# Optimization experiments

Hardware: AMD Instinct MI355X
Metric: run time of the kernel (lower is better)

The kernel has to match this reference:

```python
import jax, jax.numpy as jnp
import numpy as np

BS, NQ, NC, NT = 64, 300, 10, 30
W_CLASS, W_BBOX, W_GIOU = 2.0, 5.0, 2.0


def cxcywh_to_xyxy(b):
    c, s = b[..., :2], b[..., 2:]
    return jnp.concatenate([c - 0.5 * s, c + 0.5 * s], axis=-1)


def _area(b):
    return (b[..., 2] - b[..., 0]) * (b[..., 3] - b[..., 1])


def giou_pairwise(a, b):
    # a: [N,4] xyxy, b: [M,4] xyxy -> [N,M]
    sum_area = _area(a)[:, None] + _area(b)[None, :]
    lt = jnp.maximum(a[:, None, :2], b[None, :, :2])
    rb = jnp.minimum(a[:, None, 2:], b[None, :, 2:])
    wh = jnp.clip(rb - lt, 0.0)
    inter = wh[..., 0] * wh[..., 1]
    union = sum_area - inter
    iou = inter / union
    ltc = jnp.minimum(a[:, None, :2], b[None, :, :2])
    rbc = jnp.maximum(a[:, None, 2:], b[None, :, 2:])
    whc = jnp.clip(rbc - ltc, 0.0)
    areac = whc[..., 0] * whc[..., 1]
    return iou - (areac - union) / areac


def giou_elementwise(a, b):
    # a, b: [N,4] xyxy -> [N]
    sum_area = _area(a) + _area(b)
    lt = jnp.maximum(a[..., :2], b[..., :2])
    rb = jnp.minimum(a[..., 2:], b[..., 2:])
    wh = jnp.clip(rb - lt, 0.0)
    inter = wh[..., 0] * wh[..., 1]
    union = sum_area - inter
    iou = inter / union
    ltc = jnp.minimum(a[..., :2], b[..., :2])
    rbc = jnp.maximum(a[..., 2:], b[..., 2:])
    whc = jnp.clip(rbc - ltc, 0.0)
    areac = whc[..., 0] * whc[..., 1]
    return iou - (areac - union) / areac


def hungarian(cost):
    # Exact rectangular assignment (Kuhn-Munkres with potentials), rows n <= cols m.
    # Returns (row_ind, col_ind) of the n matched pairs, equivalent to
    # scipy.optimize.linear_sum_assignment.
    n, m = cost.shape
    u = np.zeros(n + 1)
    v = np.zeros(m + 1)
    p = np.zeros(m + 1, dtype=np.int64)    # p[j] = row matched to col j (1-based)
    way = np.zeros(m + 1, dtype=np.int64)
    for i in range(1, n + 1):
        p[0] = i
        j0 = 0
        minv = np.full(m + 1, np.inf)
        used = np.zeros(m + 1, dtype=bool)
        while True:
            used[j0] = True
            i0 = p[j0]
            cur = cost[i0 - 1] - u[i0] - v[1:]
            mask = ~used[1:]
            better = mask & (cur < minv[1:])
            minv[1:] = np.where(better, cur, minv[1:])
            way[1:] = np.where(better, j0, way[1:])
            free = np.nonzero(mask)[0]
            j1 = free[np.argmin(minv[1:][free])] + 1
            delta = minv[j1]
            u[p[used]] += delta
            v[used] -= delta
            minv[~used] -= delta
            j0 = j1
            if p[j0] == 0:
                break
        while j0 != 0:
            j1 = way[j0]
            p[j0] = p[j1]
            j0 = j1
    rows = p[1:] - 1
    cols = np.arange(m)
    sel = rows >= 0
    return rows[sel], cols[sel]


def compute_match(pred_logits, pred_boxes, labels, boxes):
    # Mirrors @torch.no_grad() match(): build cost matrix on device, assign on host.
    bs, nq, _ = pred_logits.shape
    t = boxes.shape[1]
    out_prob = jax.nn.sigmoid(pred_logits).reshape(bs * nq, -1)
    out_bbox = pred_boxes.reshape(bs * nq, 4)
    tgt_ids = labels.reshape(-1)
    tgt_bbox = boxes.reshape(-1, 4)
    cost_class = -out_prob[:, tgt_ids]                                   # [bs*nq, bs*t]
    cost_bbox = jnp.sum(jnp.abs(out_bbox[:, None, :] - tgt_bbox[None, :, :]), -1)
    cost_giou = -giou_pairwise(cxcywh_to_xyxy(out_bbox), cxcywh_to_xyxy(tgt_bbox))
    C = W_BBOX * cost_bbox + W_CLASS * cost_class + W_GIOU * cost_giou
    C = np.asarray(jax.device_get(C), dtype=np.float64).reshape(bs, nq, bs * t)
    bidx, sidx, tidx = [], [], []
    for b in range(bs):
        block = C[b, :, b * t:(b + 1) * t]          # [nq, t]
        r, c = hungarian(block.T)                   # rows = targets, cols = queries
        bidx.extend([b] * len(c))
        sidx.extend(c.tolist())
        tidx.extend(r.tolist())
    return (np.asarray(bidx, np.int64), np.asarray(sidx, np.int64),
            np.asarray(tidx, np.int64))


def compute_loss(pred_logits, pred_boxes, labels, boxes, bidx, sidx, tidx):
    bs, nq, _ = pred_logits.shape
    num = max(1, len(bidx))
    target_classes = jnp.full((bs, nq), 10, dtype=jnp.int32)
    target_classes = target_classes.at[bidx, sidx].set(
        labels[bidx, tidx].astype(jnp.int32))
    onehot = jax.nn.one_hot(target_classes, 11, dtype=pred_logits.dtype)[..., :10]
    # sigmoid focal loss, alpha=0.25, gamma=2, reduction='sum'
    x, t = pred_logits, onehot
    p = jax.nn.sigmoid(x)
    ce = jnp.maximum(x, 0.0) - x * t + jnp.log1p(jnp.exp(-jnp.abs(x)))
    p_t = p * t + (1.0 - p) * (1.0 - t)
    alpha_t = 0.25 * t + 0.75 * (1.0 - t)
    loss_ce = jnp.sum(alpha_t * ce * (1.0 - p_t) ** 2) / num
    src_boxes = pred_boxes[bidx, sidx]
    tgt_boxes = boxes[bidx, tidx]
    loss_bbox = jnp.sum(jnp.abs(src_boxes - tgt_boxes)) / num
    g = giou_elementwise(cxcywh_to_xyxy(src_boxes), cxcywh_to_xyxy(tgt_boxes))
    loss_giou = jnp.sum(1.0 - g) / num
    return loss_ce + 5.0 * loss_bbox + 2.0 * loss_giou


def setup_inputs() -> dict:
    key = jax.random.key(0)
    k0, k1, k2, k3 = jax.random.split(key, 4)
    pred_logits = jax.random.normal(k0, (BS, NQ, NC), dtype=jnp.float32)
    pred_boxes = jax.random.uniform(k1, (BS, NQ, 4), dtype=jnp.float32)
    labels = jax.random.randint(k2, (BS, NT), 0, 10, dtype=jnp.int64)
    boxes = jax.random.uniform(k3, (BS, NT, 4), dtype=jnp.float32)
    return {"pred_logits": pred_logits, "pred_boxes": pred_boxes,
            "labels": labels, "boxes": boxes}


def reference(pred_logits, pred_boxes, labels, boxes):
    bidx, sidx, tidx = compute_match(pred_logits, pred_boxes, labels, boxes)
    return compute_loss(pred_logits, pred_boxes, labels, boxes, bidx, sidx, tidx)
```

## Files before the change

kernel.cpp:

```cpp
#include <hip/hip_runtime.h>
#include <math.h>

#define NQ 300
#define NQP 301
#define NT 30
#define NC 10
#define NTH 512
#define NWAVE 8
#define INFF 3.0e38f

__device__ __forceinline__ float sigf(float x){ return 1.0f/(1.0f + expf(-x)); }
__device__ __forceinline__ float softplusf(float x){ return fmaxf(x,0.0f) + log1pf(expf(-fabsf(x))); }

template<int CTRL,int RMASK>
__device__ __forceinline__ float dppmin_f(float x){
  int t = __builtin_amdgcn_update_dpp(0x7f800000, __float_as_int(x), CTRL, RMASK, 0xf, false);
  return fminf(x, __int_as_float(t));
}
template<int CTRL,int RMASK>
__device__ __forceinline__ unsigned dppmin_u(unsigned x){
  unsigned t = (unsigned)__builtin_amdgcn_update_dpp((int)0xFFFFFFFFu, (int)x, CTRL, RMASK, 0xf, false);
  return x < t ? x : t;
}
template<int CTRL,int RMASK>
__device__ __forceinline__ float dppadd_f(float x){
  int t = __builtin_amdgcn_update_dpp(0, __float_as_int(x), CTRL, RMASK, 0xf, false);
  return x + __int_as_float(t);
}
__device__ __forceinline__ void wave_argmin64(float v, unsigned idx, float &ov, int &oj){
  float x = v;
  x = dppmin_f<0x111,0xf>(x); x = dppmin_f<0x112,0xf>(x);
  x = dppmin_f<0x114,0xf>(x); x = dppmin_f<0x118,0xf>(x);
  x = dppmin_f<0x142,0xa>(x); x = dppmin_f<0x143,0xc>(x);
  float vmin = __int_as_float(__builtin_amdgcn_readlane(__float_as_int(x), 63));
  unsigned c = (v == vmin) ? idx : 0xFFFFFFFFu;
  c = dppmin_u<0x111,0xf>(c); c = dppmin_u<0x112,0xf>(c);
  c = dppmin_u<0x114,0xf>(c); c = dppmin_u<0x118,0xf>(c);
  c = dppmin_u<0x142,0xa>(c); c = dppmin_u<0x143,0xc>(c);
  oj = __builtin_amdgcn_readlane((int)c, 63);
  ov = vmin;
}
__device__ __forceinline__ float wave_sum64(float v){
  float x = v;
  x = dppadd_f<0x111,0xf>(x); x = dppadd_f<0x112,0xf>(x);
  x = dppadd_f<0x114,0xf>(x); x = dppadd_f<0x118,0xf>(x);
  x = dppadd_f<0x142,0xa>(x); x = dppadd_f<0x143,0xc>(x);
  return __int_as_float(__builtin_amdgcn_readlane(__float_as_int(x), 63));
}

__global__ __launch_bounds__(NTH) void hm_main(
    const float* __restrict__ logits,
    const float* __restrict__ pbox,
    const int*   __restrict__ labels,
    const float* __restrict__ tbox,
    float* __restrict__ out)
{
  const int b = blockIdx.x;
  const int tid = threadIdx.x;
  const int wv = tid >> 6, ln = tid & 63;

  __shared__ float D[NT*NQ];
  __shared__ float psmT[NC*NQP];
  __shared__ float qraw[NQ][4], qxy[NQ][4], qarea[NQ];
  __shared__ float traw[NT][4], txy[NT][4], tarea[NT];
  __shared__ int   tlab[NT];
  __shared__ float uu[NT+1];
  __shared__ int   pcol[NQ];
  __shared__ int   wayl[NQ];
  __shared__ int   rargm[NT];
  __shared__ float redw[NWAVE];

  const float4* pb4 = (const float4*)pbox;
  for (int q = tid; q < NQ; q += NTH) {
    float4 s = pb4[(size_t)b*NQ + q];
    qraw[q][0]=s.x; qraw[q][1]=s.y; qraw[q][2]=s.z; qraw[q][3]=s.w;
    float x0=s.x-0.5f*s.z, y0=s.y-0.5f*s.w, x1=s.x+0.5f*s.z, y1=s.y+0.5f*s.w;
    qxy[q][0]=x0; qxy[q][1]=y0; qxy[q][2]=x1; qxy[q][3]=y1;
    qarea[q]=(x1-x0)*(y1-y0);
  }
  if (tid < NT) {
    float4 s = ((const float4*)tbox)[(size_t)b*NT + tid];
    traw[tid][0]=s.x; traw[tid][1]=s.y; traw[tid][2]=s.z; traw[tid][3]=s.w;
    float x0=s.x-0.5f*s.z, y0=s.y-0.5f*s.w, x1=s.x+0.5f*s.z, y1=s.y+0.5f*s.w;
    txy[tid][0]=x0; txy[tid][1]=y0; txy[tid][2]=x1; txy[tid][3]=y1;
    tarea[tid]=(x1-x0)*(y1-y0);
    tlab[tid]=labels[b*NT + tid];
  }
  for (int j = tid; j < NQ; j += NTH) { pcol[j]=0; wayl[j]=0x7fffffff; }

  float tot = 0.f;
  for (int e = tid; e < NQ*NC; e += NTH) {
    float x = logits[(size_t)b*NQ*NC + e];
    float pr = sigf(x);
    int q = e / NC, c = e - q*NC;
    psmT[c*NQP + q] = pr;
    tot += 0.75f * softplusf(x) * pr * pr;
  }
  __syncthreads();

  for (int i = wv; i < NT; i += NWAVE) {
    const float t0=traw[i][0], t1=traw[i][1], t2=traw[i][2], t3=traw[i][3];
    const float x0=txy[i][0], y0=txy[i][1], x1=txy[i][2], y1=txy[i][3];
    const float ta=tarea[i]; const int lab=tlab[i];
    const float* prow = &psmT[lab*NQP];
    float bv=INFF; unsigned bj=0xFFFFFFFFu;
    #pragma unroll
    for (int k = 0; k < 5; ++k) {
      int q = ln + (k<<6);
      if (k < 4 || ln < (NQ-256)) {
        float cb = fabsf(qraw[q][0]-t0)+fabsf(qraw[q][1]-t1)
                 + fabsf(qraw[q][2]-t2)+fabsf(qraw[q][3]-t3);
        float lt0=fmaxf(qxy[q][0],x0), lt1=fmaxf(qxy[q][1],y0);
        float rb0=fminf(qxy[q][2],x1), rb1=fminf(qxy[q][3],y1);
        float iw=fmaxf(rb0-lt0,0.f), ih=fmaxf(rb1-lt1,0.f);
        float inter=iw*ih;
        float uni=qarea[q]+ta-inter;
        float iou=inter/uni;
        float c0=fminf(qxy[q][0],x0), c1=fminf(qxy[q][1],y0);
        float c2=fmaxf(qxy[q][2],x1), c3=fmaxf(qxy[q][3],y1);
        float cw=fmaxf(c2-c0,0.f), ch=fmaxf(c3-c1,0.f);
        float areac=cw*ch;
        float g=iou-(areac-uni)/areac;
        float dval = 5.f*cb - 2.f*prow[q] - 2.f*g;
        D[i*NQ+q] = dval;
        if (dval < bv) { bv=dval; bj=(unsigned)q; }
      }
    }
    float vmin; int jmin;
    wave_argmin64(bv, bj, vmin, jmin);
    if (ln == 0) { uu[i+1]=vmin; rargm[i]=jmin; }
  }
  __syncthreads();

  if (tid < 64) {
    const int lane = tid;
    float u_reg = (lane < NT) ? uu[lane+1] : 0.f;
    float vvr[5] = {0.f,0.f,0.f,0.f,0.f};
    const bool v4 = lane < (NQ - 256);
    int jm = (lane < NT) ? rargm[lane] : 0;
    bool winner = false;
    if (lane < NT) {
      atomicMin(&wayl[jm], lane);
      winner = (wayl[jm] == lane);
      if (winner) pcol[jm] = lane + 1;
    }
    unsigned freerows = (unsigned)__ballot(lane < NT && !winner);
    while (freerows) {
      int fr = __builtin_ctz(freerows); freerows &= (freerows - 1);
      const int it = fr + 1;
      float minvr[5] = {INFF,INFF,INFF,INFF,INFF};
      int   usedm = 0;
      bool  onpath = (lane == fr);
      int   j0 = -1, i0 = it, j1 = 0;
      for (;;) {
        float ui0 = __int_as_float(__builtin_amdgcn_readlane(__float_as_int(u_reg), i0-1));
        const float* Drow = &D[(i0-1)*NQ];
        float lval = INFF; unsigned lidx = 0xFFFFFFFFu;
        #pragma unroll
        for (int k = 0; k < 5; ++k) {
          int c = lane + (k<<6);
          if ((k < 4 || v4) && !((usedm>>k)&1)) {
            float cur = Drow[c] - ui0 - vvr[k];
            if (cur < minvr[k]) { minvr[k] = cur; wayl[c] = j0; }
            if (minvr[k] < lval) { lval = minvr[k]; lidx = (unsigned)c; }
          }
        }
        float delta; int j1i;
        wave_argmin64(lval, lidx, delta, j1i);
        j1 = j1i;
        if (onpath) u_reg += delta;
        #pragma unroll
        for (int k = 0; k < 5; ++k) {
          if ((usedm>>k)&1) vvr[k]  -= delta;
          else              minvr[k] -= delta;
        }
        int pj1 = pcol[j1];
        if (pj1 == 0) break;
        onpath = onpath || (lane == (pj1-1));
        if (lane == (j1 & 63)) usedm |= (1 << (j1 >> 6));
        j0 = j1; i0 = pj1;
      }
      int j = j1;
      for (;;) {
        int jp = wayl[j];
        int rr = (jp < 0) ? it : pcol[jp];
        pcol[j] = rr;
        if (jp < 0) break;
        j = jp;
      }
    }
  }
  __syncthreads();

  if (tid < NQ) {
    int row = pcol[tid];
    if (row > 0) {
      int ti = row-1, q = tid;
      float l1 = fabsf(qraw[q][0]-traw[ti][0]) + fabsf(qraw[q][1]-traw[ti][1])
               + fabsf(qraw[q][2]-traw[ti][2]) + fabsf(qraw[q][3]-traw[ti][3]);
      float lt0=fmaxf(qxy[q][0],txy[ti][0]), lt1=fmaxf(qxy[q][1],txy[ti][1]);
      float rb0=fminf(qxy[q][2],txy[ti][2]), rb1=fminf(qxy[q][3],txy[ti][3]);
      float iw=fmaxf(rb0-lt0,0.f), ih=fmaxf(rb1-lt1,0.f);
      float inter=iw*ih;
      float uni=qarea[q]+tarea[ti]-inter;
      float iou=inter/uni;
      float c0=fminf(qxy[q][0],txy[ti][0]), c1=fminf(qxy[q][1],txy[ti][1]);
      float c2=fmaxf(qxy[q][2],txy[ti][2]), c3=fmaxf(qxy[q][3],txy[ti][3]);
      float cw=fmaxf(c2-c0,0.f), ch=fmaxf(c3-c1,0.f);
      float areac=cw*ch;
      float g=iou-(areac-uni)/areac;
      float x  = logits[((size_t)b*NQ+q)*NC + tlab[ti]];
      float pr = psmT[tlab[ti]*NQP + q];
      float sp = softplusf(x);
      float term0 = 0.75f*sp*pr*pr;
      float term1 = 0.25f*(sp - x)*(1.f-pr)*(1.f-pr);
      tot += (term1 - term0) + 5.f*l1 + 2.f*(1.f-g);
    }
  }
  float wsum = wave_sum64(tot);
  if (ln == 0) redw[wv] = wsum;
  __syncthreads();
  if (tid == 0) {
    float s = 0.f;
    #pragma unroll
    for (int w = 0; w < NWAVE; ++w) s += redw[w];
    atomicAdd(out, s * (1.0f/1920.0f));
  }
}

extern "C" void kernel_launch(void* const* d_in, const int* in_sizes, int n_in,
                              void* d_out, int out_size, void* d_ws, size_t ws_size,
                              hipStream_t stream) {
  const float* logits = (const float*)d_in[0];
  const float* pbox   = (const float*)d_in[1];
  const int*   labels = (const int*)d_in[2];
  const float* tbox   = (const float*)d_in[3];
  hipMemsetAsync(d_out, 0, sizeof(float), stream);
  hm_main<<<dim3(64), dim3(NTH), 0, stream>>>(logits, pbox, labels, tbox, (float*)d_out);
}
```

Measured before the change: 27.10 us.

## Keep Hungarian column state and query boxes in registers instead of LDS

Query boxes are now loaded straight into per-lane registers (five slots per lane) rather than staged in shared memory. The single-wave Hungarian solver keeps the column-to-row assignment and back-pointer arrays in registers, reading them across lanes with readlane. This is meant to remove LDS round-trips from the serial augmenting-path loop, which dominates latency. The costs are higher register pressure and switch-based slot selection, and the final loss pass is remapped so each wave handles one query slot.

```diff
diff --git a/kernel.cpp b/kernel.cpp
--- a/kernel.cpp
+++ b/kernel.cpp
@@ -11,6 +11,12 @@
 
 __device__ __forceinline__ float sigf(float x){ return 1.0f/(1.0f + expf(-x)); }
 __device__ __forceinline__ float softplusf(float x){ return fmaxf(x,0.0f) + log1pf(expf(-fabsf(x))); }
+__device__ __forceinline__ float readlane_f(float v, int l){
+  return __int_as_float(__builtin_amdgcn_readlane(__float_as_int(v), l));
+}
+__device__ __forceinline__ int readlane_i(int v, int l){
+  return __builtin_amdgcn_readlane(v, l);
+}
 
 template<int CTRL,int RMASK>
 __device__ __forceinline__ float dppmin_f(float x){
@@ -61,22 +67,27 @@
 
   __shared__ float D[NT*NQ];
   __shared__ float psmT[NC*NQP];
-  __shared__ float qraw[NQ][4], qxy[NQ][4], qarea[NQ];
   __shared__ float traw[NT][4], txy[NT][4], tarea[NT];
   __shared__ int   tlab[NT];
   __shared__ float uu[NT+1];
   __shared__ int   pcol[NQ];
-  __shared__ int   wayl[NQ];
+  __shared__ int   claimA[NQ];
   __shared__ int   rargm[NT];
   __shared__ float redw[NWAVE];
 
-  const float4* pb4 = (const float4*)pbox;
-  for (int q = tid; q < NQ; q += NTH) {
-    float4 s = pb4[(size_t)b*NQ + q];
-    qraw[q][0]=s.x; qraw[q][1]=s.y; qraw[q][2]=s.z; qraw[q][3]=s.w;
-    float x0=s.x-0.5f*s.z, y0=s.y-0.5f*s.w, x1=s.x+0.5f*s.z, y1=s.y+0.5f*s.w;
-    qxy[q][0]=x0; qxy[q][1]=y0; qxy[q][2]=x1; qxy[q][3]=y1;
-    qarea[q]=(x1-x0)*(y1-y0);
+  const bool v4 = ln < (NQ - 256);
+
+  float qcx[5],qcy[5],qw[5],qh[5],qx0[5],qy0[5],qx1[5],qy1[5],qar[5];
+  {
+    const float4* pb4 = (const float4*)pbox + (size_t)b*NQ;
+    #pragma unroll
+    for (int k = 0; k < 5; ++k) {
+      float4 s = (k < 4 || v4) ? pb4[ln + (k<<6)] : make_float4(0.f,0.f,0.f,0.f);
+      qcx[k]=s.x; qcy[k]=s.y; qw[k]=s.z; qh[k]=s.w;
+      qx0[k]=s.x-0.5f*s.z; qy0[k]=s.y-0.5f*s.w;
+      qx1[k]=s.x+0.5f*s.z; qy1[k]=s.y+0.5f*s.w;
+      qar[k]=(qx1[k]-qx0[k])*(qy1[k]-qy0[k]);
+    }
   }
   if (tid < NT) {
     float4 s = ((const float4*)tbox)[(size_t)b*NT + tid];
@@ -86,7 +97,7 @@
     tarea[tid]=(x1-x0)*(y1-y0);
     tlab[tid]=labels[b*NT + tid];
   }
-  for (int j = tid; j < NQ; j += NTH) { pcol[j]=0; wayl[j]=0x7fffffff; }
+  for (int j = tid; j < NQ; j += NTH) { pcol[j]=0; claimA[j]=0x7fffffff; }
 
   float tot = 0.f;
   for (int e = tid; e < NQ*NC; e += NTH) {
@@ -101,23 +112,22 @@
   for (int i = wv; i < NT; i += NWAVE) {
     const float t0=traw[i][0], t1=traw[i][1], t2=traw[i][2], t3=traw[i][3];
     const float x0=txy[i][0], y0=txy[i][1], x1=txy[i][2], y1=txy[i][3];
-    const float ta=tarea[i]; const int lab=tlab[i];
-    const float* prow = &psmT[lab*NQP];
+    const float ta=tarea[i];
+    const float* prow = &psmT[tlab[i]*NQP];
     float bv=INFF; unsigned bj=0xFFFFFFFFu;
     #pragma unroll
     for (int k = 0; k < 5; ++k) {
-      int q = ln + (k<<6);
-      if (k < 4 || ln < (NQ-256)) {
-        float cb = fabsf(qraw[q][0]-t0)+fabsf(qraw[q][1]-t1)
-                 + fabsf(qraw[q][2]-t2)+fabsf(qraw[q][3]-t3);
-        float lt0=fmaxf(qxy[q][0],x0), lt1=fmaxf(qxy[q][1],y0);
-        float rb0=fminf(qxy[q][2],x1), rb1=fminf(qxy[q][3],y1);
+      if (k < 4 || v4) {
+        int q = ln + (k<<6);
+        float cb = fabsf(qcx[k]-t0)+fabsf(qcy[k]-t1)+fabsf(qw[k]-t2)+fabsf(qh[k]-t3);
+        float lt0=fmaxf(qx0[k],x0), lt1=fmaxf(qy0[k],y0);
+        float rb0=fminf(qx1[k],x1), rb1=fminf(qy1[k],y1);
         float iw=fmaxf(rb0-lt0,0.f), ih=fmaxf(rb1-lt1,0.f);
         float inter=iw*ih;
-        float uni=qarea[q]+ta-inter;
+        float uni=qar[k]+ta-inter;
         float iou=inter/uni;
-        float c0=fminf(qxy[q][0],x0), c1=fminf(qxy[q][1],y0);
-        float c2=fmaxf(qxy[q][2],x1), c3=fmaxf(qxy[q][3],y1);
+        float c0=fminf(qx0[k],x0), c1=fminf(qy0[k],y0);
+        float c2=fmaxf(qx1[k],x1), c3=fmaxf(qy1[k],y1);
         float cw=fmaxf(c2-c0,0.f), ch=fmaxf(c3-c1,0.f);
         float areac=cw*ch;
         float g=iou-(areac-uni)/areac;
@@ -132,89 +142,125 @@
   }
   __syncthreads();
 
-  if (tid < 64) {
-    const int lane = tid;
+  if (wv == 0) {
+    const int lane = ln;
     float u_reg = (lane < NT) ? uu[lane+1] : 0.f;
-    float vvr[5] = {0.f,0.f,0.f,0.f,0.f};
-    const bool v4 = lane < (NQ - 256);
+    float vv0=0.f,vv1=0.f,vv2=0.f,vv3=0.f,vv4=0.f;
     int jm = (lane < NT) ? rargm[lane] : 0;
     bool winner = false;
     if (lane < NT) {
-      atomicMin(&wayl[jm], lane);
-      winner = (wayl[jm] == lane);
+      atomicMin(&claimA[jm], lane);
+      winner = (claimA[jm] == lane);
       if (winner) pcol[jm] = lane + 1;
     }
     unsigned freerows = (unsigned)__ballot(lane < NT && !winner);
+    int pc0=pcol[lane], pc1=pcol[lane+64], pc2=pcol[lane+128], pc3=pcol[lane+192];
+    int pc4 = v4 ? pcol[lane+256] : 0;
+    int wy0=0, wy1=0, wy2=0, wy3=0, wy4=0;
+
     while (freerows) {
       int fr = __builtin_ctz(freerows); freerows &= (freerows - 1);
       const int it = fr + 1;
-      float minvr[5] = {INFF,INFF,INFF,INFF,INFF};
-      int   usedm = 0;
-      bool  onpath = (lane == fr);
-      int   j0 = -1, i0 = it, j1 = 0;
+      float mn0=INFF,mn1=INFF,mn2=INFF,mn3=INFF,mn4=INFF;
+      int usedm = 0;
+      bool onpath = (lane == fr);
+      int j0 = -1, i0 = it, j1 = 0;
       for (;;) {
-        float ui0 = __int_as_float(__builtin_amdgcn_readlane(__float_as_int(u_reg), i0-1));
+        float ui0 = readlane_f(u_reg, i0-1);
         const float* Drow = &D[(i0-1)*NQ];
         float lval = INFF; unsigned lidx = 0xFFFFFFFFu;
-        #pragma unroll
-        for (int k = 0; k < 5; ++k) {
-          int c = lane + (k<<6);
-          if ((k < 4 || v4) && !((usedm>>k)&1)) {
-            float cur = Drow[c] - ui0 - vvr[k];
-            if (cur < minvr[k]) { minvr[k] = cur; wayl[c] = j0; }
-            if (minvr[k] < lval) { lval = minvr[k]; lidx = (unsigned)c; }
+        #define SCAN_K(K, MN, VV, WY) \
+          if ((K < 4 || v4) && !((usedm>>K)&1)) { \
+            float cur = Drow[lane + (K<<6)] - ui0 - VV; \
+            if (cur < MN) { MN = cur; WY = j0; } \
+            if (MN < lval) { lval = MN; lidx = (unsigned)(lane + (K<<6)); } \
           }
-        }
+        SCAN_K(0, mn0, vv0, wy0)
+        SCAN_K(1, mn1, vv1, wy1)
+        SCAN_K(2, mn2, vv2, wy2)
+        SCAN_K(3, mn3, vv3, wy3)
+        SCAN_K(4, mn4, vv4, wy4)
+        #undef SCAN_K
         float delta; int j1i;
         wave_argmin64(lval, lidx, delta, j1i);
         j1 = j1i;
         if (onpath) u_reg += delta;
-        #pragma unroll
-        for (int k = 0; k < 5; ++k) {
-          if ((usedm>>k)&1) vvr[k]  -= delta;
-          else              minvr[k] -= delta;
-        }
-        int pj1 = pcol[j1];
+        #define UPD_K(K, MN, VV) if ((usedm>>K)&1) VV -= delta; else MN -= delta;
+        UPD_K(0, mn0, vv0) UPD_K(1, mn1, vv1) UPD_K(2, mn2, vv2)
+        UPD_K(3, mn3, vv3) UPD_K(4, mn4, vv4)
+        #undef UPD_K
+        int slot = j1 >> 6, src = j1 & 63;
+        int pv;
+        switch (slot) { case 0: pv=pc0; break; case 1: pv=pc1; break;
+                        case 2: pv=pc2; break; case 3: pv=pc3; break; default: pv=pc4; }
+        int pj1 = readlane_i(pv, src);
         if (pj1 == 0) break;
         onpath = onpath || (lane == (pj1-1));
-        if (lane == (j1 & 63)) usedm |= (1 << (j1 >> 6));
+        if (lane == src) usedm |= (1 << slot);
         j0 = j1; i0 = pj1;
       }
       int j = j1;
       for (;;) {
-        int jp = wayl[j];
-        int rr = (jp < 0) ? it : pcol[jp];
-        pcol[j] = rr;
+        int slot = j >> 6, src = j & 63;
+        int wval;
+        switch (slot) { case 0: wval=wy0; break; case 1: wval=wy1; break;
+                        case 2: wval=wy2; break; case 3: wval=wy3; break; default: wval=wy4; }
+        int jp = readlane_i(wval, src);
+        int rr;
+        if (jp < 0) rr = it;
+        else {
+          int s2 = jp >> 6, l2 = jp & 63;
+          int pv2;
+          switch (s2) { case 0: pv2=pc0; break; case 1: pv2=pc1; break;
+                        case 2: pv2=pc2; break; case 3: pv2=pc3; break; default: pv2=pc4; }
+          rr = readlane_i(pv2, l2);
+        }
+        switch (slot) {
+          case 0: if (lane==src) pc0=rr; break;
+          case 1: if (lane==src) pc1=rr; break;
+          case 2: if (lane==src) pc2=rr; break;
+          case 3: if (lane==src) pc3=rr; break;
+          default: if (lane==src) pc4=rr; break;
+        }
         if (jp < 0) break;
         j = jp;
       }
     }
-  }
-  __syncthreads();
-
-  if (tid < NQ) {
-    int row = pcol[tid];
+    pcol[lane]=pc0; pcol[lane+64]=pc1; pcol[lane+128]=pc2; pcol[lane+192]=pc3;
+    if (v4) pcol[lane+256]=pc4;
+  }
+  __syncthreads();
+
+  if (wv < 5 && (wv < 4 || v4)) {
+    int q = ln + (wv<<6);
+    int row = pcol[q];
     if (row > 0) {
-      int ti = row-1, q = tid;
-      float l1 = fabsf(qraw[q][0]-traw[ti][0]) + fabsf(qraw[q][1]-traw[ti][1])
-               + fabsf(qraw[q][2]-traw[ti][2]) + fabsf(qraw[q][3]-traw[ti][3]);
-      float lt0=fmaxf(qxy[q][0],txy[ti][0]), lt1=fmaxf(qxy[q][1],txy[ti][1]);
-      float rb0=fminf(qxy[q][2],txy[ti][2]), rb1=fminf(qxy[q][3],txy[ti][3]);
+      int ti = row-1;
+      float scx,scy,sw,sh,sx0,sy0,sx1,sy1,sar;
+      switch (wv) {
+        case 0: scx=qcx[0];scy=qcy[0];sw=qw[0];sh=qh[0];sx0=qx0[0];sy0=qy0[0];sx1=qx1[0];sy1=qy1[0];sar=qar[0]; break;
+        case 1: scx=qcx[1];scy=qcy[1];sw=qw[1];sh=qh[1];sx0=qx0[1];sy0=qy0[1];sx1=qx1[1];sy1=qy1[1];sar=qar[1]; break;
+        case 2: scx=qcx[2];scy=qcy[2];sw=qw[2];sh=qh[2];sx0=qx0[2];sy0=qy0[2];sx1=qx1[2];sy1=qy1[2];sar=qar[2]; break;
+        case 3: scx=qcx[3];scy=qcy[3];sw=qw[3];sh=qh[3];sx0=qx0[3];sy0=qy0[3];sx1=qx1[3];sy1=qy1[3];sar=qar[3]; break;
+        default: scx=qcx[4];scy=qcy[4];sw=qw[4];sh=qh[4];sx0=qx0[4];sy0=qy0[4];sx1=qx1[4];sy1=qy1[4];sar=qar[4]; break;
+      }
+      float l1 = fabsf(scx-traw[ti][0])+fabsf(scy-traw[ti][1])
+               + fabsf(sw -traw[ti][2])+fabsf(sh -traw[ti][3]);
+      float lt0=fmaxf(sx0,txy[ti][0]), lt1=fmaxf(sy0,txy[ti][1]);
+      float rb0=fminf(sx1,txy[ti][2]), rb1=fminf(sy1,txy[ti][3]);
       float iw=fmaxf(rb0-lt0,0.f), ih=fmaxf(rb1-lt1,0.f);
       float inter=iw*ih;
-      float uni=qarea[q]+tarea[ti]-inter;
+      float uni=sar+tarea[ti]-inter;
       float iou=inter/uni;
-      float c0=fminf(qxy[q][0],txy[ti][0]), c1=fminf(qxy[q][1],txy[ti][1]);
-      float c2=fmaxf(qxy[q][2],txy[ti][2]), c3=fmaxf(qxy[q][3],txy[ti][3]);
+      float c0=fminf(sx0,txy[ti][0]), c1=fminf(sy0,txy[ti][1]);
+      float c2=fmaxf(sx1,txy[ti][2]), c3=fmaxf(sy1,txy[ti][3]);
       float cw=fmaxf(c2-c0,0.f), ch=fmaxf(c3-c1,0.f);
       float areac=cw*ch;
       float g=iou-(areac-uni)/areac;
       float x  = logits[((size_t)b*NQ+q)*NC + tlab[ti]];
       float pr = psmT[tlab[ti]*NQP + q];
       float sp = softplusf(x);
-      float term0 = 0.75f*sp*pr*pr;
-      float term1 = 0.25f*(sp - x)*(1.f-pr)*(1.f-pr);
-      tot += (term1 - term0) + 5.f*l1 + 2.f*(1.f-g);
+      tot += (0.25f*(sp - x)*(1.f-pr)*(1.f-pr) - 0.75f*sp*pr*pr) + 5.f*l1 + 2.f*(1.f-g);
     }
   }
   float wsum = wave_sum64(tot);
```

Result: slower. 28.65 us (+5.7%).
